# Optimization experiments

Measured on AMD Instinct MI355X. Metric: run time of the kernel, lower is better.

## Reference

```python
import jax, jax.numpy as jnp
import numpy as np

B, S1, S2, H1, H2, HID = 8, 512, 512, 128, 128, 128

def setup_inputs() -> dict:
    key = jax.random.key(0)
    ks = jax.random.split(key, 8)
    return {
        "query": jax.random.normal(ks[0], (B, S1, H1), jnp.float32),
        "key": jax.random.normal(ks[1], (B, S2, H2), jnp.float32),
        "value": jax.random.normal(ks[2], (B, S2, H2), jnp.float32),
        "q_mask": jax.random.randint(ks[3], (B, S1), 0, 2, jnp.int32),
        "k_mask": jax.random.randint(ks[4], (B, S2), 0, 2, jnp.int32),
        # init_weights: Linear weight ~ N(0, 0.01), bias = 0
        "W1": jax.random.normal(ks[5], (HID, H1 + H2), jnp.float32) * 0.01,
        "b1": jnp.zeros((HID,), jnp.float32),
        "W2": jax.random.normal(ks[6], (1, HID), jnp.float32) * 0.01,
        "b2": jnp.zeros((1,), jnp.float32),
    }

def reference(query, key, value, q_mask, k_mask, W1, b1, W2, b2):
    h1 = query.shape[-1]
    # Linear on concat([q,k]) == q @ W1[:, :h1].T + k @ W1[:, h1:].T + b1
    qp = jnp.einsum('bsd,hd->bsh', query, W1[:, :h1]) + b1   # [B,S1,HID]
    kp = jnp.einsum('btd,hd->bth', key, W1[:, h1:])          # [B,S2,HID]
    h = jax.nn.relu(qp[:, :, None, :] + kp[:, None, :, :])   # [B,S1,S2,HID]
    s = jnp.einsum('bsth,h->bst', h, W2[0]) + b2[0]          # [B,S1,S2]
    mask = (q_mask[:, :, None] * k_mask[:, None, :]) > 0     # [B,S1,S2]
    A = jnp.where(mask, jnp.exp(s), 0.0)                     # masked_fill(-inf).exp()
    A_sum = jnp.clip(jnp.sum(A, axis=-1, keepdims=True), 2e-15, None)
    attn = A / A_sum
    return jnp.einsum('bst,btd->bsd', attn, value)           # [B,S1,H2]
```

## Files before the change

kernel.cpp:

```cpp
#include <hip/hip_runtime.h>

#define S 512
#define H 128
#define NROW 4096
#define TI 4

typedef _Float16 h2v __attribute__((ext_vector_type(2)));
#define BCH(x) __builtin_bit_cast(h2v, (x))

__global__ __launch_bounds__(256) void proj_kernel(
    const float* __restrict__ query, const float* __restrict__ key,
    const float* __restrict__ W1, const float* __restrict__ b1,
    const float* __restrict__ W2,
    unsigned* __restrict__ qph, unsigned* __restrict__ kph,
    unsigned* __restrict__ w2h)
{
  __shared__ float w1t[64][130];
  const int bid = blockIdx.x;
  const int tid = threadIdx.x;
  const bool isq = bid < 512;
  const float* __restrict__ src = isq ? query : key;
  const int rbase = (isq ? bid : bid - 512) * 8;
  const int off = isq ? 0 : 128;

  if (bid == 0 && tid < 64) {
    h2v p;
    p.x = (_Float16)W2[2 * tid];
    p.y = (_Float16)W2[2 * tid + 1];
    w2h[tid] = __builtin_bit_cast(unsigned, p);
  }

  const int w = __builtin_amdgcn_readfirstlane(tid >> 6);
  const int lane = tid & 63;
  const int r0 = rbase + w * 2;

  float acc[2][2];
  float2 bv = make_float2(0.f, 0.f);
  if (isq) bv = *(const float2*)(b1 + 2 * lane);
  acc[0][0] = bv.x; acc[0][1] = bv.y;
  acc[1][0] = bv.x; acc[1][1] = bv.y;

  for (int p = 0; p < 2; p++) {
    for (int idx = tid; idx < 128 * 16; idx += 256) {
      const int d4 = idx & 15, h = idx >> 4;
      const float4 v = *(const float4*)(W1 + h * 256 + off + p * 64 + d4 * 4);
      w1t[d4 * 4 + 0][h] = v.x;
      w1t[d4 * 4 + 1][h] = v.y;
      w1t[d4 * 4 + 2][h] = v.z;
      w1t[d4 * 4 + 3][h] = v.w;
    }
    __syncthreads();

    for (int dc = 0; dc < 64; dc += 8) {
      float qs[2][8];
      #pragma unroll
      for (int r = 0; r < 2; r++) {
        const float* sp = src + (size_t)(r0 + r) * H + p * 64 + dc;
        #pragma unroll
        for (int u = 0; u < 8; u++) qs[r][u] = sp[u];
      }
      #pragma unroll
      for (int dd = 0; dd < 8; dd++) {
        const float2 wv = *(const float2*)&w1t[dc + dd][2 * lane];
        #pragma unroll
        for (int r = 0; r < 2; r++) {
          acc[r][0] = __builtin_fmaf(qs[r][dd], wv.x, acc[r][0]);
          acc[r][1] = __builtin_fmaf(qs[r][dd], wv.y, acc[r][1]);
        }
      }
    }
    __syncthreads();
  }

  unsigned* __restrict__ dst = isq ? qph : kph;
  #pragma unroll
  for (int r = 0; r < 2; r++) {
    h2v p;
    p.x = (_Float16)acc[r][0];
    p.y = (_Float16)acc[r][1];
    dst[(size_t)(r0 + r) * 64 + lane] = __builtin_bit_cast(unsigned, p);
  }
}

__global__ __launch_bounds__(512, 6) void attn_kernel(
    const unsigned* __restrict__ qph, const unsigned* __restrict__ kph,
    const unsigned* __restrict__ w2h, const float* __restrict__ value,
    const int* __restrict__ q_mask, const int* __restrict__ k_mask,
    const float* __restrict__ b2, float* __restrict__ out)
{
  union __align__(16) SMU {
    float aT[8][64][12];
    float numk[8][TI][132];
  };
  __shared__ SMU sm;
  __shared__ float denk[8][TI];

  const int bid = blockIdx.x;
  const int it = (bid & 7) * 128 + (bid >> 3);
  const int r0 = it * TI;
  const int b = r0 >> 9;
  const int tid = threadIdx.x;
  const int w = __builtin_amdgcn_readfirstlane(tid >> 6);
  const int lane = tid & 63;
  const int jl = (w << 6) + lane;
  const int jg = (b << 9) + jl;
  const int km = k_mask[jg];
  const unsigned* __restrict__ kprow = kph + (size_t)jg * 64;
  const float b2v = b2[0];
  const h2v hz = {};

  float s[TI];
  #pragma unroll
  for (int i = 0; i < TI; i++) s[i] = 0.f;

  for (int hc = 0; hc < 64; hc += 16) {
    h2v kr[16];
    {
      const uint4* k4 = (const uint4*)(kprow + hc);
      const uint4 a0 = k4[0], a1 = k4[1], a2 = k4[2], a3 = k4[3];
      kr[0]  = BCH(a0.x); kr[1]  = BCH(a0.y); kr[2]  = BCH(a0.z); kr[3]  = BCH(a0.w);
      kr[4]  = BCH(a1.x); kr[5]  = BCH(a1.y); kr[6]  = BCH(a1.z); kr[7]  = BCH(a1.w);
      kr[8]  = BCH(a2.x); kr[9]  = BCH(a2.y); kr[10] = BCH(a2.z); kr[11] = BCH(a2.w);
      kr[12] = BCH(a3.x); kr[13] = BCH(a3.y); kr[14] = BCH(a3.z); kr[15] = BCH(a3.w);
    }
    h2v w2c[16];
    #pragma unroll
    for (int u = 0; u < 16; u++) w2c[u] = BCH(w2h[hc + u]);

    #pragma unroll
    for (int i = 0; i < TI; i++) {
      const unsigned* __restrict__ qrow =
          qph + (size_t)(r0 + i) * 64 + hc;
      unsigned qu[16];
      #pragma unroll
      for (int u = 0; u < 16; u++) qu[u] = qrow[u];
      #pragma unroll
      for (int u = 0; u < 16; u++) {
        h2v t = BCH(qu[u]) + kr[u];
        t = __builtin_elementwise_max(t, hz);
        s[i] = __builtin_amdgcn_fdot2(t, w2c[u], s[i], false);
      }
    }
  }

  float a[TI];
  #pragma unroll
  for (int i = 0; i < TI; i++) {
    const int qm = q_mask[r0 + i];
    a[i] = (km > 0 && qm > 0) ? __expf(s[i] + b2v) : 0.f;
  }
  #pragma unroll
  for (int i = 0; i < TI; i++) {
    float d = a[i];
    #pragma unroll
    for (int m = 32; m >= 1; m >>= 1) d += __shfl_xor(d, m, 64);
    if (lane == 0) denk[w][i] = d;
  }
  *(float4*)&sm.aT[w][lane][0] = make_float4(a[0], a[1], a[2], a[3]);
  __syncthreads();

  const int lj = lane >> 5, lh = lane & 31;
  float nr[TI][4];
  #pragma unroll
  for (int i = 0; i < TI; i++) { nr[i][0]=0.f; nr[i][1]=0.f; nr[i][2]=0.f; nr[i][3]=0.f; }
  const float* __restrict__ vbase =
      value + ((size_t)b * S + (w << 6)) * H;

  #pragma unroll 4
  for (int js = 0; js < 32; js++) {
    const int j = js * 2 + lj;
    const float4 vv = *(const float4*)(vbase + (size_t)j * H + lh * 4);
    float av[TI];
    { const float4 t0 = *(const float4*)&sm.aT[w][j][0];
      av[0]=t0.x; av[1]=t0.y; av[2]=t0.z; av[3]=t0.w; }
    #pragma unroll
    for (int i = 0; i < TI; i++) {
      nr[i][0] = __builtin_fmaf(av[i], vv.x, nr[i][0]);
      nr[i][1] = __builtin_fmaf(av[i], vv.y, nr[i][1]);
      nr[i][2] = __builtin_fmaf(av[i], vv.z, nr[i][2]);
      nr[i][3] = __builtin_fmaf(av[i], vv.w, nr[i][3]);
    }
  }
  #pragma unroll
  for (int i = 0; i < TI; i++) {
    #pragma unroll
    for (int k = 0; k < 4; k++) nr[i][k] += __shfl_xor(nr[i][k], 32, 64);
  }

  __syncthreads();
  if (lane < 32) {
    #pragma unroll
    for (int i = 0; i < TI; i++)
      *(float4*)&sm.numk[w][i][lane * 4] =
          make_float4(nr[i][0], nr[i][1], nr[i][2], nr[i][3]);
  }
  __syncthreads();

  const int ii = tid >> 7;
  const int h0 = tid & 127;
  float nx = 0.f, d = 0.f;
  #pragma unroll
  for (int ww = 0; ww < 8; ww++) {
    nx += sm.numk[ww][ii][h0];
    d += denk[ww][ii];
  }
  const float inv = 1.f / fmaxf(d, 2e-15f);
  out[(size_t)(r0 + ii) * H + h0] = nx * inv;
}

extern "C" void kernel_launch(void* const* d_in, const int* in_sizes, int n_in,
                              void* d_out, int out_size, void* d_ws, size_t ws_size,
                              hipStream_t stream)
{
  (void)in_sizes; (void)n_in; (void)out_size; (void)ws_size;
  const float* query  = (const float*)d_in[0];
  const float* key    = (const float*)d_in[1];
  const float* value  = (const float*)d_in[2];
  const int*   q_mask = (const int*)d_in[3];
  const int*   k_mask = (const int*)d_in[4];
  const float* W1     = (const float*)d_in[5];
  const float* b1     = (const float*)d_in[6];
  const float* W2     = (const float*)d_in[7];
  const float* b2     = (const float*)d_in[8];
  float* out = (float*)d_out;

  unsigned* ws  = (unsigned*)d_ws;
  unsigned* qph = ws;
  unsigned* kph = ws + (size_t)NROW * 64;
  unsigned* w2h = kph + (size_t)NROW * 64;

  proj_kernel<<<1024, 256, 0, stream>>>(query, key, W1, b1, W2, qph, kph, w2h);
  attn_kernel<<<1024, 512, 0, stream>>>(qph, kph, w2h, value, q_mask, k_mask,
                                        b2, out);
}
```

Before: 115.0 us.

## Skip masked query rows, raise rows per block to 8, pack value to fp16

Each attention block now handles 8 query rows instead of 4, which halves the grid and reuses each loaded key row across more queries. Query rows whose mask is zero skip the score computation, and the whole PV loop is skipped when all 8 rows are masked. The value tensor is converted to packed fp16 in extra blocks of the projection kernel, halving the bytes read in the PV loop. The risks are more registers per thread (occupancy hint lowered from 6 to 4), reduced value precision, and divergent branches.

```diff
diff --git a/kernel.cpp b/kernel.cpp
--- a/kernel.cpp
+++ b/kernel.cpp
@@ -3,31 +3,46 @@
 #define S 512
 #define H 128
 #define NROW 4096
-#define TI 4
+#define TI 8
 
 typedef _Float16 h2v __attribute__((ext_vector_type(2)));
 #define BCH(x) __builtin_bit_cast(h2v, (x))
 
+static __device__ __forceinline__ unsigned pkh(float a, float b) {
+  h2v p; p.x = (_Float16)a; p.y = (_Float16)b;
+  return __builtin_bit_cast(unsigned, p);
+}
+
 __global__ __launch_bounds__(256) void proj_kernel(
     const float* __restrict__ query, const float* __restrict__ key,
+    const float* __restrict__ value,
     const float* __restrict__ W1, const float* __restrict__ b1,
     const float* __restrict__ W2,
     unsigned* __restrict__ qph, unsigned* __restrict__ kph,
-    unsigned* __restrict__ w2h)
+    unsigned* __restrict__ vph, unsigned* __restrict__ w2h)
 {
   __shared__ float w1t[64][130];
   const int bid = blockIdx.x;
   const int tid = threadIdx.x;
+
+  if (bid >= 1024) {
+    const int base = (bid - 1024) * 2048 + tid * 8;
+    const float4 v0 = *(const float4*)(value + base);
+    const float4 v1 = *(const float4*)(value + base + 4);
+    uint4 o;
+    o.x = pkh(v0.x, v0.y); o.y = pkh(v0.z, v0.w);
+    o.z = pkh(v1.x, v1.y); o.w = pkh(v1.z, v1.w);
+    *(uint4*)(vph + (base >> 1)) = o;
+    return;
+  }
+
   const bool isq = bid < 512;
   const float* __restrict__ src = isq ? query : key;
   const int rbase = (isq ? bid : bid - 512) * 8;
   const int off = isq ? 0 : 128;
 
   if (bid == 0 && tid < 64) {
-    h2v p;
-    p.x = (_Float16)W2[2 * tid];
-    p.y = (_Float16)W2[2 * tid + 1];
-    w2h[tid] = __builtin_bit_cast(unsigned, p);
+    w2h[tid] = pkh(W2[2 * tid], W2[2 * tid + 1]);
   }
 
   const int w = __builtin_amdgcn_readfirstlane(tid >> 6);
@@ -74,17 +89,13 @@
 
   unsigned* __restrict__ dst = isq ? qph : kph;
   #pragma unroll
-  for (int r = 0; r < 2; r++) {
-    h2v p;
-    p.x = (_Float16)acc[r][0];
-    p.y = (_Float16)acc[r][1];
-    dst[(size_t)(r0 + r) * 64 + lane] = __builtin_bit_cast(unsigned, p);
-  }
-}
-
-__global__ __launch_bounds__(512, 6) void attn_kernel(
+  for (int r = 0; r < 2; r++)
+    dst[(size_t)(r0 + r) * 64 + lane] = pkh(acc[r][0], acc[r][1]);
+}
+
+__global__ __launch_bounds__(512, 4) void attn_kernel(
     const unsigned* __restrict__ qph, const unsigned* __restrict__ kph,
-    const unsigned* __restrict__ w2h, const float* __restrict__ value,
+    const unsigned* __restrict__ w2h, const unsigned* __restrict__ vph,
     const int* __restrict__ q_mask, const int* __restrict__ k_mask,
     const float* __restrict__ b2, float* __restrict__ out)
 {
@@ -96,7 +107,7 @@
   __shared__ float denk[8][TI];
 
   const int bid = blockIdx.x;
-  const int it = (bid & 7) * 128 + (bid >> 3);
+  const int it = (bid & 7) * 64 + (bid >> 3);
   const int r0 = it * TI;
   const int b = r0 >> 9;
   const int tid = threadIdx.x;
@@ -109,82 +120,100 @@
   const float b2v = b2[0];
   const h2v hz = {};
 
+  int qmv[TI];
+  int anyq = 0;
+  #pragma unroll
+  for (int i = 0; i < TI; i++) { qmv[i] = q_mask[r0 + i]; anyq |= qmv[i]; }
+
   float s[TI];
   #pragma unroll
   for (int i = 0; i < TI; i++) s[i] = 0.f;
 
-  for (int hc = 0; hc < 64; hc += 16) {
-    h2v kr[16];
-    {
-      const uint4* k4 = (const uint4*)(kprow + hc);
-      const uint4 a0 = k4[0], a1 = k4[1], a2 = k4[2], a3 = k4[3];
-      kr[0]  = BCH(a0.x); kr[1]  = BCH(a0.y); kr[2]  = BCH(a0.z); kr[3]  = BCH(a0.w);
-      kr[4]  = BCH(a1.x); kr[5]  = BCH(a1.y); kr[6]  = BCH(a1.z); kr[7]  = BCH(a1.w);
-      kr[8]  = BCH(a2.x); kr[9]  = BCH(a2.y); kr[10] = BCH(a2.z); kr[11] = BCH(a2.w);
-      kr[12] = BCH(a3.x); kr[13] = BCH(a3.y); kr[14] = BCH(a3.z); kr[15] = BCH(a3.w);
-    }
-    h2v w2c[16];
-    #pragma unroll
-    for (int u = 0; u < 16; u++) w2c[u] = BCH(w2h[hc + u]);
-
+  if (anyq) {
+    for (int hc = 0; hc < 64; hc += 16) {
+      h2v kr[16];
+      {
+        const uint4* k4 = (const uint4*)(kprow + hc);
+        const uint4 a0 = k4[0], a1 = k4[1], a2 = k4[2], a3 = k4[3];
+        kr[0]  = BCH(a0.x); kr[1]  = BCH(a0.y); kr[2]  = BCH(a0.z); kr[3]  = BCH(a0.w);
+        kr[4]  = BCH(a1.x); kr[5]  = BCH(a1.y); kr[6]  = BCH(a1.z); kr[7]  = BCH(a1.w);
+        kr[8]  = BCH(a2.x); kr[9]  = BCH(a2.y); kr[10] = BCH(a2.z); kr[11] = BCH(a2.w);
+        kr[12] = BCH(a3.x); kr[13] = BCH(a3.y); kr[14] = BCH(a3.z); kr[15] = BCH(a3.w);
+      }
+      h2v w2c[16];
+      #pragma unroll
+      for (int u = 0; u < 16; u++) w2c[u] = BCH(w2h[hc + u]);
+
+      #pragma unroll
+      for (int i = 0; i < TI; i++) {
+        if (qmv[i]) {
+          const unsigned* __restrict__ qrow =
+              qph + (size_t)(r0 + i) * 64 + hc;
+          unsigned qu[16];
+          #pragma unroll
+          for (int u = 0; u < 16; u++) qu[u] = qrow[u];
+          #pragma unroll
+          for (int u = 0; u < 16; u++) {
+            h2v t = BCH(qu[u]) + kr[u];
+            t = __builtin_elementwise_max(t, hz);
+            s[i] = __builtin_amdgcn_fdot2(t, w2c[u], s[i], false);
+          }
+        }
+      }
+    }
+  }
+
+  float a[TI];
+  #pragma unroll
+  for (int i = 0; i < TI; i++) {
+    if (qmv[i]) {
+      a[i] = (km > 0) ? __expf(s[i] + b2v) : 0.f;
+      float d = a[i];
+      #pragma unroll
+      for (int m = 32; m >= 1; m >>= 1) d += __shfl_xor(d, m, 64);
+      if (lane == 0) denk[w][i] = d;
+    } else {
+      a[i] = 0.f;
+      if (lane == 0) denk[w][i] = 0.f;
+    }
+  }
+  *(float4*)&sm.aT[w][lane][0] = make_float4(a[0], a[1], a[2], a[3]);
+  *(float4*)&sm.aT[w][lane][4] = make_float4(a[4], a[5], a[6], a[7]);
+  __syncthreads();
+
+  const int lj = lane >> 5, lh = lane & 31;
+  float nr[TI][4];
+  #pragma unroll
+  for (int i = 0; i < TI; i++) { nr[i][0]=0.f; nr[i][1]=0.f; nr[i][2]=0.f; nr[i][3]=0.f; }
+  const unsigned* __restrict__ vbase =
+      vph + ((size_t)b * S + (w << 6)) * 64;
+
+  if (anyq) {
+    #pragma unroll 4
+    for (int js = 0; js < 32; js++) {
+      const int j = js * 2 + lj;
+      const uint2 vv = *(const uint2*)(vbase + (size_t)j * 64 + lh * 2);
+      const h2v p0 = BCH(vv.x), p1 = BCH(vv.y);
+      const float v0 = (float)p0.x, v1 = (float)p0.y;
+      const float v2 = (float)p1.x, v3 = (float)p1.y;
+      float av[TI];
+      { const float4 t0 = *(const float4*)&sm.aT[w][j][0];
+        const float4 t1 = *(const float4*)&sm.aT[w][j][4];
+        av[0]=t0.x; av[1]=t0.y; av[2]=t0.z; av[3]=t0.w;
+        av[4]=t1.x; av[5]=t1.y; av[6]=t1.z; av[7]=t1.w; }
+      #pragma unroll
+      for (int i = 0; i < TI; i++) {
+        nr[i][0] = __builtin_fmaf(av[i], v0, nr[i][0]);
+        nr[i][1] = __builtin_fmaf(av[i], v1, nr[i][1]);
+        nr[i][2] = __builtin_fmaf(av[i], v2, nr[i][2]);
+        nr[i][3] = __builtin_fmaf(av[i], v3, nr[i][3]);
+      }
+    }
     #pragma unroll
     for (int i = 0; i < TI; i++) {
-      const unsigned* __restrict__ qrow =
-          qph + (size_t)(r0 + i) * 64 + hc;
-      unsigned qu[16];
-      #pragma unroll
-      for (int u = 0; u < 16; u++) qu[u] = qrow[u];
-      #pragma unroll
-      for (int u = 0; u < 16; u++) {
-        h2v t = BCH(qu[u]) + kr[u];
-        t = __builtin_elementwise_max(t, hz);
-        s[i] = __builtin_amdgcn_fdot2(t, w2c[u], s[i], false);
-      }
-    }
-  }
-
-  float a[TI];
-  #pragma unroll
-  for (int i = 0; i < TI; i++) {
-    const int qm = q_mask[r0 + i];
-    a[i] = (km > 0 && qm > 0) ? __expf(s[i] + b2v) : 0.f;
-  }
-  #pragma unroll
-  for (int i = 0; i < TI; i++) {
-    float d = a[i];
-    #pragma unroll
-    for (int m = 32; m >= 1; m >>= 1) d += __shfl_xor(d, m, 64);
-    if (lane == 0) denk[w][i] = d;
-  }
-  *(float4*)&sm.aT[w][lane][0] = make_float4(a[0], a[1], a[2], a[3]);
-  __syncthreads();
-
-  const int lj = lane >> 5, lh = lane & 31;
-  float nr[TI][4];
-  #pragma unroll
-  for (int i = 0; i < TI; i++) { nr[i][0]=0.f; nr[i][1]=0.f; nr[i][2]=0.f; nr[i][3]=0.f; }
-  const float* __restrict__ vbase =
-      value + ((size_t)b * S + (w << 6)) * H;
-
-  #pragma unroll 4
-  for (int js = 0; js < 32; js++) {
-    const int j = js * 2 + lj;
-    const float4 vv = *(const float4*)(vbase + (size_t)j * H + lh * 4);
-    float av[TI];
-    { const float4 t0 = *(const float4*)&sm.aT[w][j][0];
-      av[0]=t0.x; av[1]=t0.y; av[2]=t0.z; av[3]=t0.w; }
-    #pragma unroll
-    for (int i = 0; i < TI; i++) {
-      nr[i][0] = __builtin_fmaf(av[i], vv.x, nr[i][0]);
-      nr[i][1] = __builtin_fmaf(av[i], vv.y, nr[i][1]);
-      nr[i][2] = __builtin_fmaf(av[i], vv.z, nr[i][2]);
-      nr[i][3] = __builtin_fmaf(av[i], vv.w, nr[i][3]);
-    }
-  }
-  #pragma unroll
-  for (int i = 0; i < TI; i++) {
-    #pragma unroll
-    for (int k = 0; k < 4; k++) nr[i][k] += __shfl_xor(nr[i][k], 32, 64);
+      #pragma unroll
+      for (int k = 0; k < 4; k++) nr[i][k] += __shfl_xor(nr[i][k], 32, 64);
+    }
   }
 
   __syncthreads();
@@ -196,16 +225,18 @@
   }
   __syncthreads();
 
-  const int ii = tid >> 7;
-  const int h0 = tid & 127;
-  float nx = 0.f, d = 0.f;
+  const int ii = tid >> 6;
+  const int h0 = tid & 63;
+  float n0 = 0.f, n1 = 0.f, d = 0.f;
   #pragma unroll
   for (int ww = 0; ww < 8; ww++) {
-    nx += sm.numk[ww][ii][h0];
+    n0 += sm.numk[ww][ii][h0];
+    n1 += sm.numk[ww][ii][h0 + 64];
     d += denk[ww][ii];
   }
   const float inv = 1.f / fmaxf(d, 2e-15f);
-  out[(size_t)(r0 + ii) * H + h0] = nx * inv;
+  out[(size_t)(r0 + ii) * H + h0] = n0 * inv;
+  out[(size_t)(r0 + ii) * H + h0 + 64] = n1 * inv;
 }
 
 extern "C" void kernel_launch(void* const* d_in, const int* in_sizes, int n_in,
@@ -227,9 +258,11 @@
   unsigned* ws  = (unsigned*)d_ws;
   unsigned* qph = ws;
   unsigned* kph = ws + (size_t)NROW * 64;
-  unsigned* w2h = kph + (size_t)NROW * 64;
-
-  proj_kernel<<<1024, 256, 0, stream>>>(query, key, W1, b1, W2, qph, kph, w2h);
-  attn_kernel<<<1024, 512, 0, stream>>>(qph, kph, w2h, value, q_mask, k_mask,
-                                        b2, out);
-}
+  unsigned* vph = kph + (size_t)NROW * 64;
+  unsigned* w2h = vph + (size_t)NROW * 64;
+
+  proj_kernel<<<1280, 256, 0, stream>>>(query, key, value, W1, b1, W2,
+                                        qph, kph, vph, w2h);
+  attn_kernel<<<512, 512, 0, stream>>>(qph, kph, w2h, vph, q_mask, k_mask,
+                                       b2, out);
+}
```

After: 106.6 us. -7.3%, faster.
